# Kernel tuning notes

Measured on AMD Instinct MI355X. Metric: run time of the kernel, lower is better.

The kernel has to match this reference:

```python
import jax, jax.numpy as jnp
import numpy as np

N, T, C, H = 32, 512, 768, 1536  # batch, seq_len, dim, int(dim*expand)


def setup_inputs() -> dict:
    key = jax.random.key(0)
    ks = jax.random.split(key, 10)
    sc = lambda fan: 1.0 / np.sqrt(fan)
    return {
        "x_seq": jax.random.normal(ks[0], (N, T, C), jnp.float32),
        "sup_seq": jax.random.uniform(ks[1], (N, T, 1), jnp.float32),
        # torch nn.Linear weights are [out, in]; y = x @ W.T + b
        "W_in": jax.random.normal(ks[2], (C, C), jnp.float32) * sc(C),
        "W_out": jax.random.normal(ks[3], (C, C), jnp.float32) * sc(C),
        "W_bg": jax.random.normal(ks[4], (C, C), jnp.float32) * sc(C),
        "b_bg": jax.random.normal(ks[5], (C,), jnp.float32) * 0.01,
        "W_sg": jax.random.normal(ks[6], (C, 1), jnp.float32),
        "b_sg": jax.random.normal(ks[7], (C,), jnp.float32) * 0.01,
        "W_f1": jax.random.normal(ks[8], (H, C), jnp.float32) * sc(C),
        "b_f1": jnp.zeros((H,), jnp.float32),
        "W_f2": jax.random.normal(ks[9], (C, H), jnp.float32) * sc(H),
        "b_f2": jnp.zeros((C,), jnp.float32),
    }


def reference(x_seq, sup_seq, W_in, W_out, W_bg, b_bg, W_sg, b_sg, W_f1, b_f1, W_f2, b_f2):
    # in_proj (no bias)
    x = jnp.einsum('ntc,dc->ntd', x_seq, W_in)                      # [N,T,C]
    # per-step FFN with residual (exact erf GELU, matching torch default)
    h = jax.nn.gelu(jnp.einsum('ntc,hc->nth', x, W_f1) + b_f1, approximate=False)
    xt = x + jnp.einsum('nth,ch->ntc', h, W_f2) + b_f2              # [N,T,C]
    # input-dependent gate (base_gate * sup_to_gate)
    g = jax.nn.sigmoid(jnp.einsum('ntc,dc->ntd', xt, W_bg) + b_bg)
    g = g * jax.nn.sigmoid(jnp.einsum('nto,do->ntd', sup_seq, W_sg) + b_sg)
    # linear recurrence s_t = (1-g_t)*s_{t-1} + g_t*xt_t, s_0 = 0 -> associative scan
    a = 1.0 - g
    b = g * xt

    def combine(c1, c2):
        a1, b1 = c1
        a2, b2 = c2
        return a2 * a1, a2 * b1 + b2

    _, s = jax.lax.associative_scan(combine, (a, b), axis=1)        # [N,T,C]
    return jnp.einsum('ntc,dc->ntd', s, W_out)
```

## Files before the change

### kernel.cpp

```cpp
#include <hip/hip_runtime.h>
#include <hip/hip_bf16.h>
#include <math.h>

typedef __bf16 bf16;
typedef __attribute__((ext_vector_type(8))) __bf16 bf16x8;
typedef __attribute__((ext_vector_type(4))) __bf16 bf16x4;
typedef __attribute__((ext_vector_type(4))) float f32x4;

constexpr int BM = 128, BN = 128, BK = 32;

enum { EPI_PLAIN = 0, EPI_GELU = 1, EPI_RES = 2, EPI_GATE = 3 };

__device__ __forceinline__ void async16(const void* g, void* l) {
  __builtin_amdgcn_global_load_lds(
      (const __attribute__((address_space(1))) void*)g,
      (__attribute__((address_space(3))) void*)l, 16, 0, 0);
}

template <typename CT, int EPI>
__global__ __launch_bounds__(256, 2) void gemm_bt_a(
    const bf16* __restrict__ A, const bf16* __restrict__ B, CT* __restrict__ C,
    const float* __restrict__ bias, const bf16* __restrict__ resid,
    const float* __restrict__ sup, const float* __restrict__ wsg,
    const float* __restrict__ bsg, int M, int N, int K) {
  __shared__ bf16 As[BM * BK];
  __shared__ bf16 Bs[BN * BK];

  const int tid = threadIdx.x;
  const int bm = blockIdx.x, bn = blockIdx.y;
  const int lane = tid & 63;
  const int wv = tid >> 6;
  const int wm = (wv >> 1) * 64, wn = (wv & 1) * 64;
  const int quad = lane >> 4, l16 = lane & 15;

  f32x4 acc[4][4];
#pragma unroll
  for (int i = 0; i < 4; i++)
#pragma unroll
    for (int j = 0; j < 4; j++) acc[i][j] = f32x4{0.f, 0.f, 0.f, 0.f};

  const bf16* Ab = A + (size_t)(bm * BM) * K;
  const bf16* Bb = B + (size_t)(bn * BN) * K;
  const int srow = tid >> 2, sk8 = (tid & 3) * 8;

  for (int kk = 0; kk < K; kk += BK) {
#pragma unroll
    for (int it = 0; it < 2; ++it) {
      int row = it * 64 + srow;
      async16(Ab + (size_t)row * K + kk + sk8, &As[(it * 256 + wv * 64) * 8]);
    }
#pragma unroll
    for (int it = 0; it < 2; ++it) {
      int row = it * 64 + srow;
      async16(Bb + (size_t)row * K + kk + sk8, &Bs[(it * 256 + wv * 64) * 8]);
    }
    __syncthreads();

    bf16x8 af[4], bfr[4];
#pragma unroll
    for (int i = 0; i < 4; i++) af[i] = *(const bf16x8*)&As[(wm + i * 16 + l16) * BK + quad * 8];
#pragma unroll
    for (int j = 0; j < 4; j++) bfr[j] = *(const bf16x8*)&Bs[(wn + j * 16 + l16) * BK + quad * 8];
#pragma unroll
    for (int i = 0; i < 4; i++)
#pragma unroll
      for (int j = 0; j < 4; j++)
        acc[i][j] = __builtin_amdgcn_mfma_f32_16x16x32_bf16(af[i], bfr[j], acc[i][j], 0, 0, 0);
    __syncthreads();
  }

#pragma unroll
  for (int i = 0; i < 4; i++) {
    int row0 = bm * BM + wm + i * 16 + quad * 4;
#pragma unroll
    for (int j = 0; j < 4; j++) {
      int col = bn * BN + wn + j * 16 + l16;
#pragma unroll
      for (int r = 0; r < 4; r++) {
        int row = row0 + r;
        size_t idx = (size_t)row * N + col;
        float v = acc[i][j][r];
        if constexpr (EPI == EPI_PLAIN) {
          C[idx] = (CT)v;
        } else if constexpr (EPI == EPI_GELU) {
          v += bias[col];
          float gl = 0.5f * v * (1.0f + erff(v * 0.70710678118654752f));
          C[idx] = (CT)gl;
        } else if constexpr (EPI == EPI_RES) {
          v += bias[col] + (float)resid[idx];
          C[idx] = (CT)v;
        } else {
          v += bias[col];
          float g1 = 1.0f / (1.0f + expf(-v));
          float z = sup[row] * wsg[col] + bsg[col];
          float g2 = 1.0f / (1.0f + expf(-z));
          C[idx] = (CT)(g1 * g2);
        }
      }
    }
  }
}

constexpr int SC_CH = 32, SC_NCH = 16, SC_CW = 32;

__global__ __launch_bounds__(512) void scan2_kernel(const float* __restrict__ g,
                                                    const bf16* __restrict__ xt,
                                                    bf16* __restrict__ s, int T, int C) {
  __shared__ float lA[SC_NCH][SC_CW];
  __shared__ float lB[SC_NCH][SC_CW];
  __shared__ float lC[SC_NCH][SC_CW];
  const int cl = threadIdx.x & (SC_CW - 1);
  const int ch = threadIdx.x / SC_CW;
  const int c = blockIdx.x * SC_CW + cl;
  const int n = blockIdx.y;
  const size_t base = ((size_t)n * T + ch * SC_CH) * C + c;

  float a_arr[SC_CH], sl[SC_CH];
  float A = 1.f, B = 0.f;
#pragma unroll
  for (int t = 0; t < SC_CH; ++t) {
    size_t idx = base + (size_t)t * C;
    float gv = g[idx], xv = (float)xt[idx];
    float at = 1.0f - gv;
    a_arr[t] = at;
    B = at * B + gv * xv;
    sl[t] = B;
    A *= at;
  }
  lA[ch][cl] = A;
  lB[ch][cl] = B;
  __syncthreads();
  if (ch == 0) {
    float carry = 0.f;
#pragma unroll
    for (int j = 0; j < SC_NCH; ++j) {
      lC[j][cl] = carry;
      carry = lA[j][cl] * carry + lB[j][cl];
    }
  }
  __syncthreads();
  const float carry = lC[ch][cl];
  float P = 1.f;
#pragma unroll
  for (int t = 0; t < SC_CH; ++t) {
    P *= a_arr[t];
    s[base + (size_t)t * C] = (bf16)(sl[t] + P * carry);
  }
}

__global__ __launch_bounds__(256) void cvt5_kernel(
    const float* s0, bf16* d0, int n0, const float* s1, bf16* d1, int n1,
    const float* s2, bf16* d2, int n2, const float* s3, bf16* d3, int n3,
    const float* s4, bf16* d4, int n4) {
  const float* s; bf16* d; int n;
  switch (blockIdx.y) {
    case 0: s = s0; d = d0; n = n0; break;
    case 1: s = s1; d = d1; n = n1; break;
    case 2: s = s2; d = d2; n = n2; break;
    case 3: s = s3; d = d3; n = n3; break;
    default: s = s4; d = d4; n = n4; break;
  }
  int i = blockIdx.x * 256 + threadIdx.x;
  if (i < n) d[i] = (bf16)s[i];
}

__global__ __launch_bounds__(256) void cvtx_kernel(const float* __restrict__ in,
                                                   bf16* __restrict__ out, int n4) {
  int i = blockIdx.x * 256 + threadIdx.x;
  if (i < n4) {
    f32x4 v = *(const f32x4*)(in + (size_t)i * 4);
    bf16x4 b;
    b[0] = (bf16)v[0]; b[1] = (bf16)v[1]; b[2] = (bf16)v[2]; b[3] = (bf16)v[3];
    *(bf16x4*)(out + (size_t)i * 4) = b;
  }
}

extern "C" void kernel_launch(void* const* d_in, const int* in_sizes, int n_in,
                              void* d_out, int out_size, void* d_ws, size_t ws_size,
                              hipStream_t stream) {
  const float* x_seq = (const float*)d_in[0];
  const float* sup = (const float*)d_in[1];
  const float* W_in = (const float*)d_in[2];
  const float* W_out = (const float*)d_in[3];
  const float* W_bg = (const float*)d_in[4];
  const float* b_bg = (const float*)d_in[5];
  const float* W_sg = (const float*)d_in[6];
  const float* b_sg = (const float*)d_in[7];
  const float* W_f1 = (const float*)d_in[8];
  const float* b_f1 = (const float*)d_in[9];
  const float* W_f2 = (const float*)d_in[10];
  const float* b_f2 = (const float*)d_in[11];

  const int Nb = 32, T = 512, C = 768, H = 1536;
  const int M = Nb * T;

  char* ws = (char*)d_ws;
  size_t off = 0;
  auto alloc = [&](size_t bytes) {
    void* p = ws + off;
    off += (bytes + 255) & ~(size_t)255;
    return p;
  };
  bf16* Win_bf = (bf16*)alloc((size_t)C * C * 2);
  bf16* Wf1_bf = (bf16*)alloc((size_t)H * C * 2);
  bf16* Wf2_bf = (bf16*)alloc((size_t)C * H * 2);
  bf16* Wbg_bf = (bf16*)alloc((size_t)C * C * 2);
  bf16* Wout_bf = (bf16*)alloc((size_t)C * C * 2);
  bf16* xs_bf = (bf16*)alloc((size_t)M * C * 2);
  bf16* x_bf = (bf16*)alloc((size_t)M * C * 2);
  bf16* h_bf = (bf16*)alloc((size_t)M * H * 2);
  bf16* xt_bf = (bf16*)alloc((size_t)M * C * 2);
  float* g_f = (float*)alloc((size_t)M * C * 4);
  bf16* s_bf = x_bf;

  cvt5_kernel<<<dim3((H * C + 255) / 256, 5), 256, 0, stream>>>(
      W_in, Win_bf, C * C, W_f1, Wf1_bf, H * C, W_f2, Wf2_bf, C * H,
      W_bg, Wbg_bf, C * C, W_out, Wout_bf, C * C);
  cvtx_kernel<<<(M * C / 4 + 255) / 256, 256, 0, stream>>>(x_seq, xs_bf, M * C / 4);

  dim3 blk(256);
  gemm_bt_a<bf16, EPI_PLAIN><<<dim3(M / BM, C / BN), blk, 0, stream>>>(
      xs_bf, Win_bf, x_bf, nullptr, nullptr, nullptr, nullptr, nullptr, M, C, C);
  gemm_bt_a<bf16, EPI_GELU><<<dim3(M / BM, H / BN), blk, 0, stream>>>(
      x_bf, Wf1_bf, h_bf, b_f1, nullptr, nullptr, nullptr, nullptr, M, H, C);
  gemm_bt_a<bf16, EPI_RES><<<dim3(M / BM, C / BN), blk, 0, stream>>>(
      h_bf, Wf2_bf, xt_bf, b_f2, x_bf, nullptr, nullptr, nullptr, M, C, H);
  gemm_bt_a<float, EPI_GATE><<<dim3(M / BM, C / BN), blk, 0, stream>>>(
      xt_bf, Wbg_bf, g_f, b_bg, nullptr, sup, W_sg, b_sg, M, C, C);
  scan2_kernel<<<dim3(C / SC_CW, Nb), dim3(SC_CW * SC_NCH), 0, stream>>>(
      g_f, xt_bf, s_bf, T, C);
  gemm_bt_a<float, EPI_PLAIN><<<dim3(M / BM, C / BN), blk, 0, stream>>>(
      s_bf, Wout_bf, (float*)d_out, nullptr, nullptr, nullptr, nullptr, nullptr, M, C, C);
}
```

Baseline: 368.2 us.

## Replace GEMM with 256x256-tile, 8-wave, multi-stage pipelined kernel with swizzled LDS

```diff
diff --git a/kernel.cpp b/kernel.cpp
--- a/kernel.cpp
+++ b/kernel.cpp
@@ -7,8 +7,6 @@
 typedef __attribute__((ext_vector_type(4))) __bf16 bf16x4;
 typedef __attribute__((ext_vector_type(4))) float f32x4;
 
-constexpr int BM = 128, BN = 128, BK = 32;
-
 enum { EPI_PLAIN = 0, EPI_GELU = 1, EPI_RES = 2, EPI_GATE = 3 };
 
 __device__ __forceinline__ void async16(const void* g, void* l) {
@@ -17,68 +15,151 @@
       (__attribute__((address_space(3))) void*)l, 16, 0, 0);
 }
 
+__device__ __forceinline__ void bar() {
+  asm volatile("" ::: "memory");
+  __builtin_amdgcn_s_barrier();
+  asm volatile("" ::: "memory");
+}
+
+#define WAIT_VM(n) asm volatile("s_waitcnt vmcnt(" #n ")" ::: "memory")
+#define MFMA16(d, va, vb) \
+  d = __builtin_amdgcn_mfma_f32_16x16x32_bf16(va, vb, d, 0, 0, 0)
+
 template <typename CT, int EPI>
-__global__ __launch_bounds__(256, 2) void gemm_bt_a(
+__global__ __launch_bounds__(512, 2) void gemm256(
     const bf16* __restrict__ A, const bf16* __restrict__ B, CT* __restrict__ C,
     const float* __restrict__ bias, const bf16* __restrict__ resid,
     const float* __restrict__ sup, const float* __restrict__ wsg,
     const float* __restrict__ bsg, int M, int N, int K) {
-  __shared__ bf16 As[BM * BK];
-  __shared__ bf16 Bs[BN * BK];
+  __shared__ bf16 As[4][8192];
+  __shared__ bf16 Bs[4][8192];
 
   const int tid = threadIdx.x;
   const int bm = blockIdx.x, bn = blockIdx.y;
-  const int lane = tid & 63;
-  const int wv = tid >> 6;
-  const int wm = (wv >> 1) * 64, wn = (wv & 1) * 64;
+  const int lane = tid & 63, wv = tid >> 6;
+  const int wm = wv >> 2, wn = wv & 3;
   const int quad = lane >> 4, l16 = lane & 15;
 
-  f32x4 acc[4][4];
-#pragma unroll
-  for (int i = 0; i < 4; i++)
+  const int slot8 = (quad ^ ((l16 >> 1) & 3)) * 8;
+  const int offA = (wm * 128 + l16) * 32 + slot8;
+  const int offB = (wn * 64 + l16) * 32 + slot8;
+
+  const int r0 = tid >> 2;
+  const int q8 = ((tid & 3) ^ ((r0 >> 1) & 3)) * 8;
+  const bf16* pA0 = A + (size_t)(bm * 256 + r0) * K + q8;
+  const bf16* pA1 = A + (size_t)(bm * 256 + r0 + 128) * K + q8;
+  const bf16* pB0 = B + (size_t)(bn * 256 + r0) * K + q8;
+  const bf16* pB1 = B + (size_t)(bn * 256 + r0 + 128) * K + q8;
+  bf16* lA0 = &As[0][0] + wv * 512;
+  bf16* lA1 = &As[0][0] + 4096 + wv * 512;
+  bf16* lB0 = &Bs[0][0] + wv * 512;
+  bf16* lB1 = &Bs[0][0] + 4096 + wv * 512;
+
+  auto stA = [&](int s, int col) {
+    async16(pA0 + col, lA0 + s * 8192);
+    async16(pA1 + col, lA1 + s * 8192);
+  };
+  auto stB = [&](int s, int col) {
+    async16(pB0 + col, lB0 + s * 8192);
+    async16(pB1 + col, lB1 + s * 8192);
+  };
+  auto ldA = [&](int s, int i) {
+    return *(const bf16x8*)(&As[s][offA + i * 512]);
+  };
+  auto ldB = [&](int s, int j) {
+    return *(const bf16x8*)(&Bs[s][offB + j * 512]);
+  };
+
+  f32x4 acc[8][4];
+#pragma unroll
+  for (int i = 0; i < 8; i++)
 #pragma unroll
     for (int j = 0; j < 4; j++) acc[i][j] = f32x4{0.f, 0.f, 0.f, 0.f};
 
-  const bf16* Ab = A + (size_t)(bm * BM) * K;
-  const bf16* Bb = B + (size_t)(bn * BN) * K;
-  const int srow = tid >> 2, sk8 = (tid & 3) * 8;
-
-  for (int kk = 0; kk < K; kk += BK) {
-#pragma unroll
-    for (int it = 0; it < 2; ++it) {
-      int row = it * 64 + srow;
-      async16(Ab + (size_t)row * K + kk + sk8, &As[(it * 256 + wv * 64) * 8]);
+  stA(0, 0);
+  stB(0, 0);
+  stA(1, 32);
+  stB(1, 32);
+  WAIT_VM(4);
+  bar();
+
+  const int nt = K >> 6;
+  for (int t = 0; t < nt; ++t) {
+    const int s0 = (t & 1) * 2, s1 = s0 + 1;
+    const int n0 = 2 - s0, n1 = n0 + 1;
+    const bool st = (t + 1) < nt;
+    const int ncol = (t + 1) * 64;
+    bf16x8 a[4], b[4];
+
+#pragma unroll
+    for (int i = 0; i < 4; i++) a[i] = ldA(s0, i);
+#pragma unroll
+    for (int j = 0; j < 4; j++) b[j] = ldB(s0, j);
+    if (st) stA(n0, ncol);
+    bar();
+    __builtin_amdgcn_s_setprio(1);
+#pragma unroll
+    for (int i = 0; i < 4; i++)
+#pragma unroll
+      for (int j = 0; j < 4; j++) MFMA16(acc[i][j], a[i], b[j]);
+    __builtin_amdgcn_s_setprio(0);
+    bar();
+
+#pragma unroll
+    for (int i = 0; i < 4; i++) a[i] = ldA(s0, i + 4);
+    if (st) stB(n0, ncol);
+    bar();
+    __builtin_amdgcn_s_setprio(1);
+#pragma unroll
+    for (int i = 0; i < 4; i++)
+#pragma unroll
+      for (int j = 0; j < 4; j++) MFMA16(acc[i + 4][j], a[i], b[j]);
+    __builtin_amdgcn_s_setprio(0);
+    if (st) {
+      WAIT_VM(4);
+    } else {
+      WAIT_VM(0);
     }
-#pragma unroll
-    for (int it = 0; it < 2; ++it) {
-      int row = it * 64 + srow;
-      async16(Bb + (size_t)row * K + kk + sk8, &Bs[(it * 256 + wv * 64) * 8]);
-    }
-    __syncthreads();
-
-    bf16x8 af[4], bfr[4];
-#pragma unroll
-    for (int i = 0; i < 4; i++) af[i] = *(const bf16x8*)&As[(wm + i * 16 + l16) * BK + quad * 8];
-#pragma unroll
-    for (int j = 0; j < 4; j++) bfr[j] = *(const bf16x8*)&Bs[(wn + j * 16 + l16) * BK + quad * 8];
+    bar();
+
+#pragma unroll
+    for (int i = 0; i < 4; i++) a[i] = ldA(s1, i);
+#pragma unroll
+    for (int j = 0; j < 4; j++) b[j] = ldB(s1, j);
+    if (st) stA(n1, ncol + 32);
+    bar();
+    __builtin_amdgcn_s_setprio(1);
 #pragma unroll
     for (int i = 0; i < 4; i++)
 #pragma unroll
-      for (int j = 0; j < 4; j++)
-        acc[i][j] = __builtin_amdgcn_mfma_f32_16x16x32_bf16(af[i], bfr[j], acc[i][j], 0, 0, 0);
-    __syncthreads();
-  }
-
-#pragma unroll
-  for (int i = 0; i < 4; i++) {
-    int row0 = bm * BM + wm + i * 16 + quad * 4;
+      for (int j = 0; j < 4; j++) MFMA16(acc[i][j], a[i], b[j]);
+    __builtin_amdgcn_s_setprio(0);
+    bar();
+
+#pragma unroll
+    for (int i = 0; i < 4; i++) a[i] = ldA(s1, i + 4);
+    if (st) stB(n1, ncol + 32);
+    bar();
+    __builtin_amdgcn_s_setprio(1);
+#pragma unroll
+    for (int i = 0; i < 4; i++)
+#pragma unroll
+      for (int j = 0; j < 4; j++) MFMA16(acc[i + 4][j], a[i], b[j]);
+    __builtin_amdgcn_s_setprio(0);
+    if (st) WAIT_VM(4);
+    bar();
+  }
+
+#pragma unroll
+  for (int i = 0; i < 8; i++) {
+    const int row0 = bm * 256 + wm * 128 + i * 16 + quad * 4;
 #pragma unroll
     for (int j = 0; j < 4; j++) {
-      int col = bn * BN + wn + j * 16 + l16;
+      const int col = bn * 256 + wn * 64 + j * 16 + l16;
 #pragma unroll
       for (int r = 0; r < 4; r++) {
-        int row = row0 + r;
-        size_t idx = (size_t)row * N + col;
+        const int row = row0 + r;
+        const size_t idx = (size_t)row * N + col;
         float v = acc[i][j][r];
         if constexpr (EPI == EPI_PLAIN) {
           C[idx] = (CT)v;
@@ -218,17 +299,17 @@
       W_bg, Wbg_bf, C * C, W_out, Wout_bf, C * C);
   cvtx_kernel<<<(M * C / 4 + 255) / 256, 256, 0, stream>>>(x_seq, xs_bf, M * C / 4);
 
-  dim3 blk(256);
-  gemm_bt_a<bf16, EPI_PLAIN><<<dim3(M / BM, C / BN), blk, 0, stream>>>(
+  dim3 blk(512);
+  gemm256<bf16, EPI_PLAIN><<<dim3(M / 256, C / 256), blk, 0, stream>>>(
       xs_bf, Win_bf, x_bf, nullptr, nullptr, nullptr, nullptr, nullptr, M, C, C);
-  gemm_bt_a<bf16, EPI_GELU><<<dim3(M / BM, H / BN), blk, 0, stream>>>(
+  gemm256<bf16, EPI_GELU><<<dim3(M / 256, H / 256), blk, 0, stream>>>(
       x_bf, Wf1_bf, h_bf, b_f1, nullptr, nullptr, nullptr, nullptr, M, H, C);
-  gemm_bt_a<bf16, EPI_RES><<<dim3(M / BM, C / BN), blk, 0, stream>>>(
+  gemm256<bf16, EPI_RES><<<dim3(M / 256, C / 256), blk, 0, stream>>>(
       h_bf, Wf2_bf, xt_bf, b_f2, x_bf, nullptr, nullptr, nullptr, M, C, H);
-  gemm_bt_a<float, EPI_GATE><<<dim3(M / BM, C / BN), blk, 0, stream>>>(
+  gemm256<float, EPI_GATE><<<dim3(M / 256, C / 256), blk, 0, stream>>>(
       xt_bf, Wbg_bf, g_f, b_bg, nullptr, sup, W_sg, b_sg, M, C, C);
   scan2_kernel<<<dim3(C / SC_CW, Nb), dim3(SC_CW * SC_NCH), 0, stream>>>(
       g_f, xt_bf, s_bf, T, C);
-  gemm_bt_a<float, EPI_PLAIN><<<dim3(M / BM, C / BN), blk, 0, stream>>>(
+  gemm256<float, EPI_PLAIN><<<dim3(M / 256, C / 256), blk, 0, stream>>>(
       s_bf, Wout_bf, (float*)d_out, nullptr, nullptr, nullptr, nullptr, nullptr, M, C, C);
 }
```

Result: slower. 413.3 us (+12.2%).

## Double-buffer GEMM LDS tiles with async prefetch and XOR-swizzled layout

Applied to the files above, without the earlier changes.

```diff
diff --git a/kernel.cpp b/kernel.cpp
--- a/kernel.cpp
+++ b/kernel.cpp
@@ -16,6 +16,14 @@
       (const __attribute__((address_space(1))) void*)g,
       (__attribute__((address_space(3))) void*)l, 16, 0, 0);
 }
+
+__device__ __forceinline__ void bar_lgkm() {
+  asm volatile("s_waitcnt lgkmcnt(0)\n\ts_barrier" ::: "memory");
+}
+
+#define WAIT_VM(n) asm volatile("s_waitcnt vmcnt(" #n ")" ::: "memory")
+#define MFMA16(d, va, vb) \
+  d = __builtin_amdgcn_mfma_f32_16x16x32_bf16(va, vb, d, 0, 0, 0)
 
 template <typename CT, int EPI>
 __global__ __launch_bounds__(256, 2) void gemm_bt_a(
@@ -23,8 +31,8 @@
     const float* __restrict__ bias, const bf16* __restrict__ resid,
     const float* __restrict__ sup, const float* __restrict__ wsg,
     const float* __restrict__ bsg, int M, int N, int K) {
-  __shared__ bf16 As[BM * BK];
-  __shared__ bf16 Bs[BN * BK];
+  __shared__ bf16 As[2][BM * BK];
+  __shared__ bf16 Bs[2][BN * BK];
 
   const int tid = threadIdx.x;
   const int bm = blockIdx.x, bn = blockIdx.y;
@@ -41,32 +49,49 @@
 
   const bf16* Ab = A + (size_t)(bm * BM) * K;
   const bf16* Bb = B + (size_t)(bn * BN) * K;
-  const int srow = tid >> 2, sk8 = (tid & 3) * 8;
-
-  for (int kk = 0; kk < K; kk += BK) {
+  const int srow = tid >> 2;
+  const int sq8 = ((tid & 3) ^ ((srow >> 1) & 3)) * 8;
+  const int slot8 = (quad ^ ((l16 >> 1) & 3)) * 8;
+
+  auto stage = [&](int buf, int kk) {
 #pragma unroll
     for (int it = 0; it < 2; ++it) {
       int row = it * 64 + srow;
-      async16(Ab + (size_t)row * K + kk + sk8, &As[(it * 256 + wv * 64) * 8]);
+      async16(Ab + (size_t)row * K + kk + sq8, &As[buf][(it * 256 + wv * 64) * 8]);
     }
 #pragma unroll
     for (int it = 0; it < 2; ++it) {
       int row = it * 64 + srow;
-      async16(Bb + (size_t)row * K + kk + sk8, &Bs[(it * 256 + wv * 64) * 8]);
-    }
-    __syncthreads();
+      async16(Bb + (size_t)row * K + kk + sq8, &Bs[buf][(it * 256 + wv * 64) * 8]);
+    }
+  };
+
+  stage(0, 0);
+
+  const int nt = K / BK;
+  for (int t = 0; t < nt; ++t) {
+    const int cur = t & 1;
+    if (t + 1 < nt) {
+      stage(cur ^ 1, (t + 1) * BK);
+      WAIT_VM(4);
+    } else {
+      WAIT_VM(0);
+    }
+    bar_lgkm();
 
     bf16x8 af[4], bfr[4];
 #pragma unroll
-    for (int i = 0; i < 4; i++) af[i] = *(const bf16x8*)&As[(wm + i * 16 + l16) * BK + quad * 8];
-#pragma unroll
-    for (int j = 0; j < 4; j++) bfr[j] = *(const bf16x8*)&Bs[(wn + j * 16 + l16) * BK + quad * 8];
+    for (int i = 0; i < 4; i++)
+      af[i] = *(const bf16x8*)&As[cur][(wm + i * 16 + l16) * BK + slot8];
+#pragma unroll
+    for (int j = 0; j < 4; j++)
+      bfr[j] = *(const bf16x8*)&Bs[cur][(wn + j * 16 + l16) * BK + slot8];
 #pragma unroll
     for (int i = 0; i < 4; i++)
 #pragma unroll
       for (int j = 0; j < 4; j++)
         acc[i][j] = __builtin_amdgcn_mfma_f32_16x16x32_bf16(af[i], bfr[j], acc[i][j], 0, 0, 0);
-    __syncthreads();
+    bar_lgkm();
   }
 
 #pragma unroll
```

Measured after the change: 375.9 us. 1.02x slower.
